# Kernel optimization log

Measured on AMD Instinct MI355X. Metric: run time of the kernel, lower is better.

Reference implementation:

```python
import jax, jax.numpy as jnp
import numpy as np

D_MODEL, NUM_HEADS, ROPE_DIM = 256, 8, 16
B_GRAPHS, N_MAX = 16, 512


def _make_batch():
    # ragged graph sizes between 256 and 512 atoms; contiguous, sorted ids
    sizes = np.array([256 + (i * 256) // 15 for i in range(B_GRAPHS)], dtype=np.int64)
    return np.repeat(np.arange(B_GRAPHS), sizes)  # total N = 6137


def setup_inputs() -> dict:
    key = jax.random.key(0)
    ks = jax.random.split(key, 6)
    batch_np = _make_batch()
    N = int(batch_np.shape[0])
    x = jax.random.normal(ks[0], (N, D_MODEL), jnp.float32)
    pos = jax.random.normal(ks[1], (N, 3), jnp.float32) * 3.0
    W_qkv = jax.random.normal(ks[2], (D_MODEL, 3 * D_MODEL), jnp.float32) / np.sqrt(D_MODEL).astype(np.float32)
    W_out = jax.random.normal(ks[3], (D_MODEL, D_MODEL), jnp.float32) / np.sqrt(D_MODEL).astype(np.float32)
    rope_freqs = jax.random.normal(ks[4], (ROPE_DIM,), jnp.float32) * 0.1
    W_rope = jax.random.normal(ks[5], (ROPE_DIM, NUM_HEADS), jnp.float32) / np.sqrt(ROPE_DIM).astype(np.float32)
    gamma = jnp.ones((D_MODEL,), jnp.float32)
    beta = jnp.zeros((D_MODEL,), jnp.float32)
    return {"x": x, "pos": pos, "batch": jnp.asarray(batch_np, jnp.int32),
            "W_qkv": W_qkv, "W_out": W_out, "rope_freqs": rope_freqs,
            "W_rope": W_rope, "gamma": gamma, "beta": beta,
            "B": B_GRAPHS, "n_max": N_MAX}


def _forward(x, pos, W_qkv, W_out, rope_freqs, W_rope, gamma, beta, batch, B, n_max):
    N, d = x.shape
    H = W_rope.shape[1]
    hd = d // H
    scale = hd ** -0.5
    # pad ragged graphs to [B, n_max] via vectorized scatter (batch is sorted)
    sizes = jax.ops.segment_sum(jnp.ones((N,), jnp.int32), batch, num_segments=B)
    offsets = jnp.concatenate([jnp.zeros((1,), jnp.int32), jnp.cumsum(sizes)[:-1].astype(jnp.int32)])
    pidx = jnp.arange(N, dtype=jnp.int32) - offsets[batch]  # position within graph
    x_pad = jnp.zeros((B, n_max, d), x.dtype).at[batch, pidx].set(x)
    pos_pad = jnp.zeros((B, n_max, 3), pos.dtype).at[batch, pidx].set(pos)
    pad = jnp.ones((B, n_max), bool).at[batch, pidx].set(False)  # True = padding
    # multi-head self-attention on scalar channel
    qkv = x_pad @ W_qkv  # [B, n, 3d]
    q, k, v = jnp.split(qkv, 3, axis=-1)
    heads = lambda t: t.reshape(B, n_max, H, hd).transpose(0, 2, 1, 3)  # [B,H,n,hd]
    q, k, v = heads(q), heads(k), heads(v)
    logits = jnp.einsum('bhid,bhjd->bhij', q, k) * scale
    # Euclidean RoPE distance bias: rope_proj(cos(|omega| * ||r_i - r_j||))
    diff = pos_pad[:, :, None, :] - pos_pad[:, None, :, :]  # [B,n,n,3]
    sq = jnp.sum(diff * diff, axis=-1)
    dist = jnp.where(sq > 0, jnp.sqrt(jnp.where(sq > 0, sq, 1.0)), 0.0)  # safe norm
    fourier = jnp.cos(dist[..., None] * jnp.abs(rope_freqs))  # [B,n,n,r]
    bias = jnp.einsum('bijr,rh->bhij', fourier, W_rope)
    pair_pad = (pad[:, :, None] | pad[:, None, :])[:, None]  # [B,1,n,n]
    bias = jnp.where(pair_pad, 0.0, bias)
    logits = jnp.where(pad[:, None, None, :], -1e9, logits + bias)
    attn = jax.nn.softmax(logits, axis=-1)
    out = jnp.einsum('bhij,bhjd->bhid', attn, v)
    out = out.transpose(0, 2, 1, 3).reshape(B, n_max, d) @ W_out
    out_flat = out[batch, pidx]  # gather back to flat node list
    # residual + LayerNorm (eps = 1e-5)
    y = x + out_flat
    mu = jnp.mean(y, axis=-1, keepdims=True)
    var = jnp.mean((y - mu) ** 2, axis=-1, keepdims=True)
    return gamma * (y - mu) * jax.lax.rsqrt(var + 1e-5) + beta


def reference(x, pos, batch, W_qkv, W_out, rope_freqs, W_rope, gamma, beta, B, n_max):
    return _forward(x, pos, W_qkv, W_out, rope_freqs, W_rope, gamma, beta, batch, B, n_max)
```

## Files before the change

### kernel.cpp

```cpp
#include <hip/hip_runtime.h>
#include <hip/hip_bf16.h>

typedef __hip_bfloat16 bf16;
typedef short bf16x8 __attribute__((ext_vector_type(8)));
typedef float f32x4 __attribute__((ext_vector_type(4)));

#define NGRAPH 16
#define QSCALE 0.17677669529663687f
#define VT_LD 8192

struct __align__(16) bf8x { bf16 v[8]; };

__device__ __forceinline__ float b2f(bf16 v) { return __bfloat162float(v); }

__device__ __forceinline__ bf16x8 ldcvt8(const float* p) {
  float4 u = *(const float4*)p, v = *(const float4*)(p + 4);
  __align__(16) bf16 tmp[8];
  tmp[0] = __float2bfloat16(u.x); tmp[1] = __float2bfloat16(u.y);
  tmp[2] = __float2bfloat16(u.z); tmp[3] = __float2bfloat16(u.w);
  tmp[4] = __float2bfloat16(v.x); tmp[5] = __float2bfloat16(v.y);
  tmp[6] = __float2bfloat16(v.z); tmp[7] = __float2bfloat16(v.w);
  return *(const bf16x8*)tmp;
}

__global__ __launch_bounds__(256) void k_pre(const float* __restrict__ Wqkv,
                                             const float* __restrict__ Wout,
                                             const int* __restrict__ batch,
                                             bf16* __restrict__ Wqkv_t,
                                             bf16* __restrict__ Wout_t,
                                             int* __restrict__ offs, int N) {
  __shared__ float ld[64][65];
  int bid = blockIdx.x, t = threadIdx.x;
  int c = t & 63, r0 = t >> 6;
  if (bid < 48) {
    int k0 = (bid & 3) * 64, n0 = (bid >> 2) * 64;
    #pragma unroll
    for (int r = r0; r < 64; r += 4) ld[r][c] = Wqkv[(size_t)(k0 + r) * 768 + n0 + c];
    __syncthreads();
    #pragma unroll
    for (int r = r0; r < 64; r += 4)
      Wqkv_t[(size_t)(n0 + r) * 256 + k0 + c] = __float2bfloat16(ld[c][r]);
  } else if (bid < 64) {
    int b2 = bid - 48;
    int k0 = (b2 & 3) * 64, n0 = (b2 >> 2) * 64;
    #pragma unroll
    for (int r = r0; r < 64; r += 4) ld[r][c] = Wout[(size_t)(k0 + r) * 256 + n0 + c];
    __syncthreads();
    #pragma unroll
    for (int r = r0; r < 64; r += 4)
      Wout_t[(size_t)(n0 + r) * 256 + k0 + c] = __float2bfloat16(ld[c][r]);
  } else {
    for (int i = t; i < N; i += 256) {
      if (i == 0) { offs[0] = 0; offs[NGRAPH] = N; }
      else if (batch[i] != batch[i - 1]) offs[batch[i]] = i;
    }
  }
}

__global__ __launch_bounds__(256) void k_gemm(const float* __restrict__ x,
                                              const bf16* __restrict__ Wqkv_t,
                                              const int* __restrict__ batch,
                                              const int* __restrict__ offs,
                                              bf16* __restrict__ QKVb,
                                              bf16* __restrict__ VT, int N) {
  __shared__ float tr[64][65];
  __shared__ int rowcol[64];
  int t = threadIdx.x;
  int w = t >> 6, l = t & 63, fr = l & 15, fq = l >> 4;
  int m0 = blockIdx.x * 64, n0 = blockIdx.y * 64;
  if (t < 64) {
    int m = m0 + t; if (m > N - 1) m = N - 1;
    int b = batch[m];
    rowcol[t] = b * 512 + (m - offs[b]);
  }
  int arow = m0 + w * 16 + fr; if (arow > N - 1) arow = N - 1;
  bf16x8 af[8];
  #pragma unroll
  for (int kt = 0; kt < 8; ++kt)
    af[kt] = ldcvt8(x + (size_t)arow * 256 + kt * 32 + fq * 8);
  #pragma unroll
  for (int p = 0; p < 3; ++p) {
    f32x4 acc[4];
    #pragma unroll
    for (int nt = 0; nt < 4; ++nt) {
      acc[nt] = (f32x4){0.f, 0.f, 0.f, 0.f};
      int brow = p * 256 + n0 + nt * 16 + fr;
      #pragma unroll
      for (int kt = 0; kt < 8; ++kt) {
        bf16x8 bf_ = *(const bf16x8*)(Wqkv_t + (size_t)brow * 256 + kt * 32 + fq * 8);
        acc[nt] = __builtin_amdgcn_mfma_f32_16x16x32_bf16(af[kt], bf_, acc[nt], 0, 0, 0);
      }
    }
    float sc = (p == 0) ? QSCALE : 1.f;
    #pragma unroll
    for (int nt = 0; nt < 4; ++nt) {
      int col = p * 256 + n0 + nt * 16 + fr;
      #pragma unroll
      for (int rr = 0; rr < 4; ++rr) {
        int m = m0 + w * 16 + fq * 4 + rr;
        if (m < N) QKVb[(size_t)m * 768 + col] = __float2bfloat16(acc[nt][rr] * sc);
      }
    }
    if (p == 2) {
      #pragma unroll
      for (int nt = 0; nt < 4; ++nt)
        #pragma unroll
        for (int rr = 0; rr < 4; ++rr)
          tr[nt * 16 + fr][w * 16 + fq * 4 + rr] = acc[nt][rr];
      __syncthreads();
      int c = t >> 2, r0 = (t & 3) * 16;
      int dg = n0 + c;
      #pragma unroll
      for (int i = 0; i < 16; ++i) {
        int r = r0 + i;
        VT[(size_t)dg * VT_LD + rowcol[r]] = __float2bfloat16(tr[c][r]);
      }
    }
  }
}

__global__ __launch_bounds__(256) void k_attn(const float* __restrict__ pos,
                                              const float* __restrict__ freqs,
                                              const float* __restrict__ Wrope,
                                              const bf16* __restrict__ QKVb,
                                              const bf16* __restrict__ VT,
                                              const int* __restrict__ offs,
                                              float* __restrict__ Op,
                                              float* __restrict__ lp, int N) {
  __shared__ __align__(16) bf16 Tg[384][8];
  __shared__ __align__(16) bf16 Sbf[2][8][64][8];
  __shared__ __align__(16) bf16 Pt[4][16][40];
  int b = blockIdx.y, jc = blockIdx.z;
  int off = offs[b], n = offs[b + 1] - off;
  int q0 = blockIdx.x * 16;
  if (q0 >= n) return;
  int t = threadIdx.x, w = t >> 6, l = t & 63, fr = l & 15, fq = l >> 4;

  for (int i = t; i < 384; i += 256) {
    float d = i * 0.125f;
    float a[8];
    #pragma unroll
    for (int h = 0; h < 8; ++h) a[h] = 0.f;
    #pragma unroll
    for (int r = 0; r < 16; ++r) {
      float cv = __cosf(d * fabsf(freqs[r]));
      #pragma unroll
      for (int h = 0; h < 8; ++h) a[h] += cv * Wrope[r * 8 + h];
    }
    __align__(16) bf16 row[8];
    #pragma unroll
    for (int h = 0; h < 8; ++h) row[h] = __float2bfloat16(a[h]);
    *(bf16x8*)&Tg[i][0] = *(const bf16x8*)row;
  }

  int h0 = w, h1 = w + 4;
  const bf16* Kb0 = QKVb + (size_t)off * 768 + 256 + h0 * 32 + fq * 8;
  const bf16* Kb1 = QKVb + (size_t)off * 768 + 256 + h1 * 32 + fq * 8;
  const bf16* Vb0 = VT + (size_t)(h0 * 32 + fr) * VT_LD + b * 512 + fq * 8;
  const bf16* Vb1 = VT + (size_t)(h1 * 32 + fr) * VT_LD + b * 512 + fq * 8;
  int qrow = q0 + fr; bool qv = qrow < n;
  size_t qoff = (size_t)(qv ? off + qrow : off) * 768 + fq * 8;
  bf16x8 aq[2];
  aq[0] = *(const bf16x8*)(QKVb + qoff + h0 * 32);
  aq[1] = *(const bf16x8*)(QKVb + qoff + h1 * 32);
  if (!qv) { aq[0] = (bf16x8){0,0,0,0,0,0,0,0}; aq[1] = aq[0]; }

  int bq = t >> 5, bj = t & 31;
  float qpx[2], qpy[2], qpz[2]; bool bqv[2];
  #pragma unroll
  for (int e = 0; e < 2; ++e) {
    int qq = q0 + bq + 8 * e; bqv[e] = qq < n;
    int a = (bqv[e] ? off + qq : off) * 3;
    qpx[e] = pos[a]; qpy[e] = pos[a + 1]; qpz[e] = pos[a + 2];
  }

  f32x4 Oa[2][2];
  Oa[0][0] = (f32x4){0.f,0.f,0.f,0.f}; Oa[0][1] = Oa[0][0];
  Oa[1][0] = Oa[0][0];                 Oa[1][1] = Oa[0][0];
  float lacc[2][4] = {{0.f,0.f,0.f,0.f},{0.f,0.f,0.f,0.f}};
  int jtiles = (n + 31) >> 5;
  int jt0 = (jtiles * jc) >> 1, jt1 = (jtiles * (jc + 1)) >> 1;

  auto produce = [&](int JT, int BUF) {
    int jg = JT * 32 + bj; bool vj = jg < n;
    int a = (vj ? off + jg : off) * 3;
    float jx = pos[a], jy = pos[a + 1], jz = pos[a + 2];
    #pragma unroll
    for (int e = 0; e < 2; ++e) {
      int q = bq + 8 * e;
      int L = (q >> 2) * 16 + (bj & 15);
      int k = (bj >> 4) * 4 + (q & 3);
      if (vj && bqv[e]) {
        float dx = qpx[e] - jx, dy = qpy[e] - jy, dz = qpz[e] - jz;
        float d = sqrtf(dx * dx + dy * dy + dz * dz);
        float fi = d * 8.0f;
        int i = (int)fi; if (i > 382) i = 382;
        float fr2 = fi - (float)i;
        bf8x t0 = *(const bf8x*)&Tg[i][0];
        bf8x t1 = *(const bf8x*)&Tg[i + 1][0];
        #pragma unroll
        for (int h = 0; h < 8; ++h) {
          float u0 = b2f(t0.v[h]);
          float bv = u0 + fr2 * (b2f(t1.v[h]) - u0);
          Sbf[BUF][h][L][k] = __float2bfloat16(bv);
        }
      } else {
        bf16 s = __float2bfloat16(vj ? 0.f : -1e30f);
        #pragma unroll
        for (int h = 0; h < 8; ++h) Sbf[BUF][h][L][k] = s;
      }
    }
  };

  bf16x8 ck[2][2], cv[2][2];
  auto loadt = [&](int JT) {
    int k0 = JT * 32 + fr, k1 = k0 + 16;
    size_t r0 = (size_t)((k0 < n) ? k0 : 0) * 768;
    size_t r1 = (size_t)((k1 < n) ? k1 : 0) * 768;
    ck[0][0] = *(const bf16x8*)(Kb0 + r0); ck[0][1] = *(const bf16x8*)(Kb0 + r1);
    ck[1][0] = *(const bf16x8*)(Kb1 + r0); ck[1][1] = *(const bf16x8*)(Kb1 + r1);
    cv[0][0] = *(const bf16x8*)(Vb0 + JT * 32);
    cv[0][1] = *(const bf16x8*)(Vb0 + (size_t)16 * VT_LD + JT * 32);
    cv[1][0] = *(const bf16x8*)(Vb1 + JT * 32);
    cv[1][1] = *(const bf16x8*)(Vb1 + (size_t)16 * VT_LD + JT * 32);
  };

  __syncthreads();
  produce(jt0, 0);
  __syncthreads();
  for (int jt = jt0; jt < jt1; ++jt) {
    int par = (jt - jt0) & 1;
    loadt(jt);
    if (jt + 1 < jt1) produce(jt + 1, par ^ 1);
    #pragma unroll
    for (int hh = 0; hh < 2; ++hh) {
      int h = w + 4 * hh;
      f32x4 z = {0.f, 0.f, 0.f, 0.f};
      f32x4 S0 = __builtin_amdgcn_mfma_f32_16x16x32_bf16(aq[hh], ck[hh][0], z, 0, 0, 0);
      f32x4 S1 = __builtin_amdgcn_mfma_f32_16x16x32_bf16(aq[hh], ck[hh][1], z, 0, 0, 0);
      bf8x bb = *(const bf8x*)&Sbf[par][h][l][0];
      #pragma unroll
      for (int k = 0; k < 8; ++k) {
        int jti = k >> 2, rr = k & 3;
        float s = (jti ? S1[rr] : S0[rr]) + b2f(bb.v[k]);
        float p = __expf(s);
        lacc[hh][rr] += p;
        Pt[w][fq * 4 + rr][jti * 16 + fr] = __float2bfloat16(p);
      }
      bf16x8 ap = *(const bf16x8*)&Pt[w][fr][fq * 8];
      Oa[hh][0] = __builtin_amdgcn_mfma_f32_16x16x32_bf16(ap, cv[hh][0], Oa[hh][0], 0, 0, 0);
      Oa[hh][1] = __builtin_amdgcn_mfma_f32_16x16x32_bf16(ap, cv[hh][1], Oa[hh][1], 0, 0, 0);
    }
    __syncthreads();
  }
  #pragma unroll
  for (int hh = 0; hh < 2; ++hh)
    #pragma unroll
    for (int rr = 0; rr < 4; ++rr) {
      #pragma unroll
      for (int m2 = 1; m2 <= 8; m2 <<= 1) lacc[hh][rr] += __shfl_xor(lacc[hh][rr], m2);
    }
  float* Opc = Op + (size_t)jc * N * 256;
  float* lpc = lp + (size_t)jc * N * 8;
  #pragma unroll
  for (int hh = 0; hh < 2; ++hh) {
    int h = w + 4 * hh;
    #pragma unroll
    for (int rr = 0; rr < 4; ++rr) {
      int row = q0 + fq * 4 + rr;
      if (row < n) {
        #pragma unroll
        for (int dh = 0; dh < 2; ++dh)
          Opc[(size_t)(off + row) * 256 + h * 32 + dh * 16 + fr] = Oa[hh][dh][rr];
        if (fr == 0) lpc[(size_t)(off + row) * 8 + h] = lacc[hh][rr];
      }
    }
  }
}

__global__ __launch_bounds__(256) void k_out_ln(const float* __restrict__ Op,
                                                const float* __restrict__ lp,
                                                const bf16* __restrict__ Bt,
                                                const float* __restrict__ x,
                                                const float* __restrict__ gamma,
                                                const float* __restrict__ beta,
                                                float* __restrict__ out, int M) {
  __shared__ float ps[4][16], pss[4][16];
  int t = threadIdx.x, w = t >> 6, l = t & 63, fr = l & 15, fq = l >> 4;
  int m0 = blockIdx.x * 16;
  int arow = m0 + fr; if (arow > M - 1) arow = M - 1;
  const float* Op0 = Op;
  const float* Op1 = Op + (size_t)M * 256;
  float linv[8];
  {
    float4 a0 = *(const float4*)(lp + (size_t)arow * 8);
    float4 a1 = *(const float4*)(lp + (size_t)arow * 8 + 4);
    float4 b0 = *(const float4*)(lp + (size_t)(M + arow) * 8);
    float4 b1 = *(const float4*)(lp + (size_t)(M + arow) * 8 + 4);
    linv[0] = 1.f / (a0.x + b0.x); linv[1] = 1.f / (a0.y + b0.y);
    linv[2] = 1.f / (a0.z + b0.z); linv[3] = 1.f / (a0.w + b0.w);
    linv[4] = 1.f / (a1.x + b1.x); linv[5] = 1.f / (a1.y + b1.y);
    linv[6] = 1.f / (a1.z + b1.z); linv[7] = 1.f / (a1.w + b1.w);
  }
  bf16x8 af[8];
  #pragma unroll
  for (int kt = 0; kt < 8; ++kt) {
    size_t o = (size_t)arow * 256 + kt * 32 + fq * 8;
    float4 u0 = *(const float4*)(Op0 + o), v0 = *(const float4*)(Op0 + o + 4);
    float4 u1 = *(const float4*)(Op1 + o), v1 = *(const float4*)(Op1 + o + 4);
    float li = linv[kt];
    __align__(16) bf16 tmp[8];
    tmp[0] = __float2bfloat16((u0.x + u1.x) * li);
    tmp[1] = __float2bfloat16((u0.y + u1.y) * li);
    tmp[2] = __float2bfloat16((u0.z + u1.z) * li);
    tmp[3] = __float2bfloat16((u0.w + u1.w) * li);
    tmp[4] = __float2bfloat16((v0.x + v1.x) * li);
    tmp[5] = __float2bfloat16((v0.y + v1.y) * li);
    tmp[6] = __float2bfloat16((v0.z + v1.z) * li);
    tmp[7] = __float2bfloat16((v0.w + v1.w) * li);
    af[kt] = *(const bf16x8*)tmp;
  }
  f32x4 acc[4];
  #pragma unroll
  for (int nt = 0; nt < 4; ++nt) {
    acc[nt] = (f32x4){0.f, 0.f, 0.f, 0.f};
    int brow = w * 64 + nt * 16 + fr;
    #pragma unroll
    for (int kt = 0; kt < 8; ++kt) {
      bf16x8 bf_ = *(const bf16x8*)(Bt + (size_t)brow * 256 + kt * 32 + fq * 8);
      acc[nt] = __builtin_amdgcn_mfma_f32_16x16x32_bf16(af[kt], bf_, acc[nt], 0, 0, 0);
    }
  }
  float y[4][4];
  #pragma unroll
  for (int rr = 0; rr < 4; ++rr) {
    int row = m0 + fq * 4 + rr;
    int rc = (row < M) ? row : (M - 1);
    float s = 0.f, ss = 0.f;
    #pragma unroll
    for (int nt = 0; nt < 4; ++nt) {
      float v = acc[nt][rr] + x[(size_t)rc * 256 + w * 64 + nt * 16 + fr];
      y[rr][nt] = v; s += v; ss += v * v;
    }
    #pragma unroll
    for (int m2 = 1; m2 <= 8; m2 <<= 1) { s += __shfl_xor(s, m2); ss += __shfl_xor(ss, m2); }
    if (fr == 0) { ps[w][fq * 4 + rr] = s; pss[w][fq * 4 + rr] = ss; }
  }
  __syncthreads();
  #pragma unroll
  for (int rr = 0; rr < 4; ++rr) {
    int row = m0 + fq * 4 + rr;
    int ri = fq * 4 + rr;
    float s = ps[0][ri] + ps[1][ri] + ps[2][ri] + ps[3][ri];
    float ss = pss[0][ri] + pss[1][ri] + pss[2][ri] + pss[3][ri];
    float mean = s * (1.f / 256.f);
    float var = ss * (1.f / 256.f) - mean * mean;
    float rstd = rsqrtf(var + 1e-5f);
    if (row < M) {
      #pragma unroll
      for (int nt = 0; nt < 4; ++nt) {
        int col = w * 64 + nt * 16 + fr;
        out[(size_t)row * 256 + col] = gamma[col] * (y[rr][nt] - mean) * rstd + beta[col];
      }
    }
  }
}

extern "C" void kernel_launch(void* const* d_in, const int* in_sizes, int n_in,
                              void* d_out, int out_size, void* d_ws, size_t ws_size,
                              hipStream_t stream) {
  (void)n_in; (void)out_size; (void)ws_size;
  const float* x     = (const float*)d_in[0];
  const float* pos   = (const float*)d_in[1];
  const int*   batch = (const int*)d_in[2];
  const float* Wqkv  = (const float*)d_in[3];
  const float* Wout  = (const float*)d_in[4];
  const float* freqs = (const float*)d_in[5];
  const float* Wrope = (const float*)d_in[6];
  const float* gamma = (const float*)d_in[7];
  const float* beta  = (const float*)d_in[8];
  float* out = (float*)d_out;

  int N = in_sizes[0] / 256;

  char* base = (char*)d_ws;
  int*   offs   = (int*)base;
  bf16*  QKVb   = (bf16*)(base + 1024);
  bf16*  VT     = (bf16*)(base + 9427456);
  bf16*  Wqkv_t = (bf16*)(base + 13621760);
  bf16*  Wout_t = (bf16*)(base + 14014976);
  float* Op     = (float*)(base + 14146048);
  float* lp     = (float*)(base + 26714624);

  int MBm = (N + 63) / 64;
  k_pre<<<65, 256, 0, stream>>>(Wqkv, Wout, batch, Wqkv_t, Wout_t, offs, N);
  k_gemm<<<dim3(MBm, 4), 256, 0, stream>>>(x, Wqkv_t, batch, offs, QKVb, VT, N);
  k_attn<<<dim3(32, NGRAPH, 2), 256, 0, stream>>>(pos, freqs, Wrope, QKVb, VT, offs, Op, lp, N);
  k_out_ln<<<(N + 15) / 16, 256, 0, stream>>>(Op, lp, Wout_t, x, gamma, beta, out, N);
}
```

Measured before the change: 179.4 us.

## Precompute RoPE bias table once, widen attention key split, shrink GEMM tiles

```diff
diff --git a/kernel.cpp b/kernel.cpp
--- a/kernel.cpp
+++ b/kernel.cpp
@@ -26,8 +26,11 @@
 __global__ __launch_bounds__(256) void k_pre(const float* __restrict__ Wqkv,
                                              const float* __restrict__ Wout,
                                              const int* __restrict__ batch,
+                                             const float* __restrict__ freqs,
+                                             const float* __restrict__ Wrope,
                                              bf16* __restrict__ Wqkv_t,
                                              bf16* __restrict__ Wout_t,
+                                             float* __restrict__ Tblg,
                                              int* __restrict__ offs, int N) {
   __shared__ float ld[64][65];
   int bid = blockIdx.x, t = threadIdx.x;
@@ -49,10 +52,26 @@
     #pragma unroll
     for (int r = r0; r < 64; r += 4)
       Wout_t[(size_t)(n0 + r) * 256 + k0 + c] = __float2bfloat16(ld[c][r]);
-  } else {
+  } else if (bid == 64) {
     for (int i = t; i < N; i += 256) {
       if (i == 0) { offs[0] = 0; offs[NGRAPH] = N; }
       else if (batch[i] != batch[i - 1]) offs[batch[i]] = i;
+    }
+  } else {
+    int i = (bid - 65) * 256 + t;
+    if (i < 384) {
+      float d = i * 0.125f;
+      float a[8];
+      #pragma unroll
+      for (int h = 0; h < 8; ++h) a[h] = 0.f;
+      #pragma unroll
+      for (int r = 0; r < 16; ++r) {
+        float cv = __cosf(d * fabsf(freqs[r]));
+        #pragma unroll
+        for (int h = 0; h < 8; ++h) a[h] += cv * Wrope[r * 8 + h];
+      }
+      #pragma unroll
+      for (int h = 0; h < 8; ++h) Tblg[i * 8 + h] = a[h];
     }
   }
 }
@@ -63,28 +82,29 @@
                                               const int* __restrict__ offs,
                                               bf16* __restrict__ QKVb,
                                               bf16* __restrict__ VT, int N) {
-  __shared__ float tr[64][65];
-  __shared__ int rowcol[64];
+  __shared__ float tr[64][33];
+  __shared__ int rowcol[32];
   int t = threadIdx.x;
   int w = t >> 6, l = t & 63, fr = l & 15, fq = l >> 4;
-  int m0 = blockIdx.x * 64, n0 = blockIdx.y * 64;
-  if (t < 64) {
+  int rh = w & 1, ch = w >> 1;
+  int m0 = blockIdx.x * 32, n0 = blockIdx.y * 64;
+  if (t < 32) {
     int m = m0 + t; if (m > N - 1) m = N - 1;
     int b = batch[m];
     rowcol[t] = b * 512 + (m - offs[b]);
   }
-  int arow = m0 + w * 16 + fr; if (arow > N - 1) arow = N - 1;
+  int arow = m0 + rh * 16 + fr; if (arow > N - 1) arow = N - 1;
   bf16x8 af[8];
   #pragma unroll
   for (int kt = 0; kt < 8; ++kt)
     af[kt] = ldcvt8(x + (size_t)arow * 256 + kt * 32 + fq * 8);
   #pragma unroll
   for (int p = 0; p < 3; ++p) {
-    f32x4 acc[4];
-    #pragma unroll
-    for (int nt = 0; nt < 4; ++nt) {
+    f32x4 acc[2];
+    #pragma unroll
+    for (int nt = 0; nt < 2; ++nt) {
       acc[nt] = (f32x4){0.f, 0.f, 0.f, 0.f};
-      int brow = p * 256 + n0 + nt * 16 + fr;
+      int brow = p * 256 + n0 + ch * 32 + nt * 16 + fr;
       #pragma unroll
       for (int kt = 0; kt < 8; ++kt) {
         bf16x8 bf_ = *(const bf16x8*)(Wqkv_t + (size_t)brow * 256 + kt * 32 + fq * 8);
@@ -93,26 +113,26 @@
     }
     float sc = (p == 0) ? QSCALE : 1.f;
     #pragma unroll
-    for (int nt = 0; nt < 4; ++nt) {
-      int col = p * 256 + n0 + nt * 16 + fr;
+    for (int nt = 0; nt < 2; ++nt) {
+      int col = p * 256 + n0 + ch * 32 + nt * 16 + fr;
       #pragma unroll
       for (int rr = 0; rr < 4; ++rr) {
-        int m = m0 + w * 16 + fq * 4 + rr;
+        int m = m0 + rh * 16 + fq * 4 + rr;
         if (m < N) QKVb[(size_t)m * 768 + col] = __float2bfloat16(acc[nt][rr] * sc);
       }
     }
     if (p == 2) {
       #pragma unroll
-      for (int nt = 0; nt < 4; ++nt)
+      for (int nt = 0; nt < 2; ++nt)
         #pragma unroll
         for (int rr = 0; rr < 4; ++rr)
-          tr[nt * 16 + fr][w * 16 + fq * 4 + rr] = acc[nt][rr];
+          tr[ch * 32 + nt * 16 + fr][rh * 16 + fq * 4 + rr] = acc[nt][rr];
       __syncthreads();
-      int c = t >> 2, r0 = (t & 3) * 16;
+      int c = t >> 2, rr0 = (t & 3) * 8;
       int dg = n0 + c;
       #pragma unroll
-      for (int i = 0; i < 16; ++i) {
-        int r = r0 + i;
+      for (int i = 0; i < 8; ++i) {
+        int r = rr0 + i;
         VT[(size_t)dg * VT_LD + rowcol[r]] = __float2bfloat16(tr[c][r]);
       }
     }
@@ -120,14 +140,13 @@
 }
 
 __global__ __launch_bounds__(256) void k_attn(const float* __restrict__ pos,
-                                              const float* __restrict__ freqs,
-                                              const float* __restrict__ Wrope,
+                                              const float* __restrict__ Tblg,
                                               const bf16* __restrict__ QKVb,
                                               const bf16* __restrict__ VT,
                                               const int* __restrict__ offs,
                                               float* __restrict__ Op,
-                                              float* __restrict__ lp, int N) {
-  __shared__ __align__(16) bf16 Tg[384][8];
+                                              float* __restrict__ lp, int N, int JC) {
+  __shared__ __align__(16) float Tgf[384][8];
   __shared__ __align__(16) bf16 Sbf[2][8][64][8];
   __shared__ __align__(16) bf16 Pt[4][16][40];
   int b = blockIdx.y, jc = blockIdx.z;
@@ -136,21 +155,11 @@
   if (q0 >= n) return;
   int t = threadIdx.x, w = t >> 6, l = t & 63, fr = l & 15, fq = l >> 4;
 
-  for (int i = t; i < 384; i += 256) {
-    float d = i * 0.125f;
-    float a[8];
-    #pragma unroll
-    for (int h = 0; h < 8; ++h) a[h] = 0.f;
-    #pragma unroll
-    for (int r = 0; r < 16; ++r) {
-      float cv = __cosf(d * fabsf(freqs[r]));
-      #pragma unroll
-      for (int h = 0; h < 8; ++h) a[h] += cv * Wrope[r * 8 + h];
-    }
-    __align__(16) bf16 row[8];
-    #pragma unroll
-    for (int h = 0; h < 8; ++h) row[h] = __float2bfloat16(a[h]);
-    *(bf16x8*)&Tg[i][0] = *(const bf16x8*)row;
+  {
+    float4* dst = (float4*)&Tgf[0][0];
+    const float4* src = (const float4*)Tblg;
+    #pragma unroll
+    for (int i = t; i < 768; i += 256) dst[i] = src[i];
   }
 
   int h0 = w, h1 = w + 4;
@@ -179,7 +188,7 @@
   Oa[1][0] = Oa[0][0];                 Oa[1][1] = Oa[0][0];
   float lacc[2][4] = {{0.f,0.f,0.f,0.f},{0.f,0.f,0.f,0.f}};
   int jtiles = (n + 31) >> 5;
-  int jt0 = (jtiles * jc) >> 1, jt1 = (jtiles * (jc + 1)) >> 1;
+  int jt0 = (jtiles * jc) / JC, jt1 = (jtiles * (jc + 1)) / JC;
 
   auto produce = [&](int JT, int BUF) {
     int jg = JT * 32 + bj; bool vj = jg < n;
@@ -196,14 +205,17 @@
         float fi = d * 8.0f;
         int i = (int)fi; if (i > 382) i = 382;
         float fr2 = fi - (float)i;
-        bf8x t0 = *(const bf8x*)&Tg[i][0];
-        bf8x t1 = *(const bf8x*)&Tg[i + 1][0];
-        #pragma unroll
-        for (int h = 0; h < 8; ++h) {
-          float u0 = b2f(t0.v[h]);
-          float bv = u0 + fr2 * (b2f(t1.v[h]) - u0);
-          Sbf[BUF][h][L][k] = __float2bfloat16(bv);
-        }
+        const float* tp = &Tgf[i][0];
+        float4 a0 = *(const float4*)tp,       a1 = *(const float4*)(tp + 4);
+        float4 c0 = *(const float4*)(tp + 8), c1 = *(const float4*)(tp + 12);
+        Sbf[BUF][0][L][k] = __float2bfloat16(a0.x + fr2 * (c0.x - a0.x));
+        Sbf[BUF][1][L][k] = __float2bfloat16(a0.y + fr2 * (c0.y - a0.y));
+        Sbf[BUF][2][L][k] = __float2bfloat16(a0.z + fr2 * (c0.z - a0.z));
+        Sbf[BUF][3][L][k] = __float2bfloat16(a0.w + fr2 * (c0.w - a0.w));
+        Sbf[BUF][4][L][k] = __float2bfloat16(a1.x + fr2 * (c1.x - a1.x));
+        Sbf[BUF][5][L][k] = __float2bfloat16(a1.y + fr2 * (c1.y - a1.y));
+        Sbf[BUF][6][L][k] = __float2bfloat16(a1.z + fr2 * (c1.z - a1.z));
+        Sbf[BUF][7][L][k] = __float2bfloat16(a1.w + fr2 * (c1.w - a1.w));
       } else {
         bf16 s = __float2bfloat16(vj ? 0.f : -1e30f);
         #pragma unroll
@@ -284,40 +296,40 @@
                                                 const float* __restrict__ x,
                                                 const float* __restrict__ gamma,
                                                 const float* __restrict__ beta,
-                                                float* __restrict__ out, int M) {
+                                                float* __restrict__ out, int M, int JC) {
   __shared__ float ps[4][16], pss[4][16];
   int t = threadIdx.x, w = t >> 6, l = t & 63, fr = l & 15, fq = l >> 4;
   int m0 = blockIdx.x * 16;
   int arow = m0 + fr; if (arow > M - 1) arow = M - 1;
-  const float* Op0 = Op;
-  const float* Op1 = Op + (size_t)M * 256;
   float linv[8];
   {
-    float4 a0 = *(const float4*)(lp + (size_t)arow * 8);
-    float4 a1 = *(const float4*)(lp + (size_t)arow * 8 + 4);
-    float4 b0 = *(const float4*)(lp + (size_t)(M + arow) * 8);
-    float4 b1 = *(const float4*)(lp + (size_t)(M + arow) * 8 + 4);
-    linv[0] = 1.f / (a0.x + b0.x); linv[1] = 1.f / (a0.y + b0.y);
-    linv[2] = 1.f / (a0.z + b0.z); linv[3] = 1.f / (a0.w + b0.w);
-    linv[4] = 1.f / (a1.x + b1.x); linv[5] = 1.f / (a1.y + b1.y);
-    linv[6] = 1.f / (a1.z + b1.z); linv[7] = 1.f / (a1.w + b1.w);
+    float ls[8] = {0.f,0.f,0.f,0.f,0.f,0.f,0.f,0.f};
+    for (int c = 0; c < JC; ++c) {
+      const float* p = lp + ((size_t)c * M + arow) * 8;
+      float4 a0 = *(const float4*)p, a1 = *(const float4*)(p + 4);
+      ls[0] += a0.x; ls[1] += a0.y; ls[2] += a0.z; ls[3] += a0.w;
+      ls[4] += a1.x; ls[5] += a1.y; ls[6] += a1.z; ls[7] += a1.w;
+    }
+    #pragma unroll
+    for (int h = 0; h < 8; ++h) linv[h] = 1.f / ls[h];
   }
   bf16x8 af[8];
   #pragma unroll
   for (int kt = 0; kt < 8; ++kt) {
     size_t o = (size_t)arow * 256 + kt * 32 + fq * 8;
-    float4 u0 = *(const float4*)(Op0 + o), v0 = *(const float4*)(Op0 + o + 4);
-    float4 u1 = *(const float4*)(Op1 + o), v1 = *(const float4*)(Op1 + o + 4);
+    float s0 = 0.f, s1 = 0.f, s2 = 0.f, s3 = 0.f, s4 = 0.f, s5 = 0.f, s6 = 0.f, s7 = 0.f;
+    for (int c = 0; c < JC; ++c) {
+      const float* p = Op + (size_t)c * M * 256 + o;
+      float4 u = *(const float4*)p, v = *(const float4*)(p + 4);
+      s0 += u.x; s1 += u.y; s2 += u.z; s3 += u.w;
+      s4 += v.x; s5 += v.y; s6 += v.z; s7 += v.w;
+    }
     float li = linv[kt];
     __align__(16) bf16 tmp[8];
-    tmp[0] = __float2bfloat16((u0.x + u1.x) * li);
-    tmp[1] = __float2bfloat16((u0.y + u1.y) * li);
-    tmp[2] = __float2bfloat16((u0.z + u1.z) * li);
-    tmp[3] = __float2bfloat16((u0.w + u1.w) * li);
-    tmp[4] = __float2bfloat16((v0.x + v1.x) * li);
-    tmp[5] = __float2bfloat16((v0.y + v1.y) * li);
-    tmp[6] = __float2bfloat16((v0.z + v1.z) * li);
-    tmp[7] = __float2bfloat16((v0.w + v1.w) * li);
+    tmp[0] = __float2bfloat16(s0 * li); tmp[1] = __float2bfloat16(s1 * li);
+    tmp[2] = __float2bfloat16(s2 * li); tmp[3] = __float2bfloat16(s3 * li);
+    tmp[4] = __float2bfloat16(s4 * li); tmp[5] = __float2bfloat16(s5 * li);
+    tmp[6] = __float2bfloat16(s6 * li); tmp[7] = __float2bfloat16(s7 * li);
     af[kt] = *(const bf16x8*)tmp;
   }
   f32x4 acc[4];
@@ -369,7 +381,7 @@
 extern "C" void kernel_launch(void* const* d_in, const int* in_sizes, int n_in,
                               void* d_out, int out_size, void* d_ws, size_t ws_size,
                               hipStream_t stream) {
-  (void)n_in; (void)out_size; (void)ws_size;
+  (void)n_in; (void)out_size;
   const float* x     = (const float*)d_in[0];
   const float* pos   = (const float*)d_in[1];
   const int*   batch = (const int*)d_in[2];
@@ -383,18 +395,21 @@
 
   int N = in_sizes[0] / 256;
 
+  int JC = (ws_size >= (size_t)41 * 1024 * 1024) ? 4 : 2;
+
   char* base = (char*)d_ws;
   int*   offs   = (int*)base;
   bf16*  QKVb   = (bf16*)(base + 1024);
   bf16*  VT     = (bf16*)(base + 9427456);
   bf16*  Wqkv_t = (bf16*)(base + 13621760);
   bf16*  Wout_t = (bf16*)(base + 14014976);
-  float* Op     = (float*)(base + 14146048);
-  float* lp     = (float*)(base + 26714624);
-
-  int MBm = (N + 63) / 64;
-  k_pre<<<65, 256, 0, stream>>>(Wqkv, Wout, batch, Wqkv_t, Wout_t, offs, N);
+  float* Tblg   = (float*)(base + 14146048);
+  float* Op     = (float*)(base + 14158336);
+  float* lp     = (float*)(base + 14158336 + (size_t)JC * N * 1024);
+
+  int MBm = (N + 31) / 32;
+  k_pre<<<67, 256, 0, stream>>>(Wqkv, Wout, batch, freqs, Wrope, Wqkv_t, Wout_t, Tblg, offs, N);
   k_gemm<<<dim3(MBm, 4), 256, 0, stream>>>(x, Wqkv_t, batch, offs, QKVb, VT, N);
-  k_attn<<<dim3(32, NGRAPH, 2), 256, 0, stream>>>(pos, freqs, Wrope, QKVb, VT, offs, Op, lp, N);
-  k_out_ln<<<(N + 15) / 16, 256, 0, stream>>>(Op, lp, Wout_t, x, gamma, beta, out, N);
-}
+  k_attn<<<dim3(32, NGRAPH, JC), 256, 0, stream>>>(pos, Tblg, QKVb, VT, offs, Op, lp, N, JC);
+  k_out_ln<<<(N + 15) / 16, 256, 0, stream>>>(Op, lp, Wout_t, x, gamma, beta, out, N, JC);
+}
```

New measurement: 182.8 us. Within noise of the previous version (+1.9%).

## Split attention keys into fixed 128-key chunks and precompute rope-bias table once

Applied to the files above, without the earlier changes.

```diff
diff --git a/kernel.cpp b/kernel.cpp
--- a/kernel.cpp
+++ b/kernel.cpp
@@ -26,8 +26,11 @@
 __global__ __launch_bounds__(256) void k_pre(const float* __restrict__ Wqkv,
                                              const float* __restrict__ Wout,
                                              const int* __restrict__ batch,
+                                             const float* __restrict__ freqs,
+                                             const float* __restrict__ Wrope,
                                              bf16* __restrict__ Wqkv_t,
                                              bf16* __restrict__ Wout_t,
+                                             bf16* __restrict__ Tbg,
                                              int* __restrict__ offs, int N) {
   __shared__ float ld[64][65];
   int bid = blockIdx.x, t = threadIdx.x;
@@ -49,10 +52,28 @@
     #pragma unroll
     for (int r = r0; r < 64; r += 4)
       Wout_t[(size_t)(n0 + r) * 256 + k0 + c] = __float2bfloat16(ld[c][r]);
-  } else {
+  } else if (bid == 64) {
     for (int i = t; i < N; i += 256) {
       if (i == 0) { offs[0] = 0; offs[NGRAPH] = N; }
       else if (batch[i] != batch[i - 1]) offs[batch[i]] = i;
+    }
+  } else {
+    int i = (bid - 65) * 256 + t;
+    if (i < 384) {
+      float d = i * 0.125f;
+      float a[8];
+      #pragma unroll
+      for (int h = 0; h < 8; ++h) a[h] = 0.f;
+      #pragma unroll
+      for (int r = 0; r < 16; ++r) {
+        float cv = __cosf(d * fabsf(freqs[r]));
+        #pragma unroll
+        for (int h = 0; h < 8; ++h) a[h] += cv * Wrope[r * 8 + h];
+      }
+      __align__(16) bf16 row[8];
+      #pragma unroll
+      for (int h = 0; h < 8; ++h) row[h] = __float2bfloat16(a[h]);
+      *(bf16x8*)(Tbg + i * 8) = *(const bf16x8*)row;
     }
   }
 }
@@ -120,8 +141,7 @@
 }
 
 __global__ __launch_bounds__(256) void k_attn(const float* __restrict__ pos,
-                                              const float* __restrict__ freqs,
-                                              const float* __restrict__ Wrope,
+                                              const bf16* __restrict__ Tbg,
                                               const bf16* __restrict__ QKVb,
                                               const bf16* __restrict__ VT,
                                               const int* __restrict__ offs,
@@ -133,25 +153,13 @@
   int b = blockIdx.y, jc = blockIdx.z;
   int off = offs[b], n = offs[b + 1] - off;
   int q0 = blockIdx.x * 16;
-  if (q0 >= n) return;
+  int jtiles = (n + 31) >> 5;
+  int chunks = (jtiles + 3) >> 2;
+  if (q0 >= n || jc >= chunks) return;
   int t = threadIdx.x, w = t >> 6, l = t & 63, fr = l & 15, fq = l >> 4;
 
-  for (int i = t; i < 384; i += 256) {
-    float d = i * 0.125f;
-    float a[8];
-    #pragma unroll
-    for (int h = 0; h < 8; ++h) a[h] = 0.f;
-    #pragma unroll
-    for (int r = 0; r < 16; ++r) {
-      float cv = __cosf(d * fabsf(freqs[r]));
-      #pragma unroll
-      for (int h = 0; h < 8; ++h) a[h] += cv * Wrope[r * 8 + h];
-    }
-    __align__(16) bf16 row[8];
-    #pragma unroll
-    for (int h = 0; h < 8; ++h) row[h] = __float2bfloat16(a[h]);
-    *(bf16x8*)&Tg[i][0] = *(const bf16x8*)row;
-  }
+  for (int i = t; i < 384; i += 256)
+    *(bf16x8*)&Tg[i][0] = *(const bf16x8*)(Tbg + i * 8);
 
   int h0 = w, h1 = w + 4;
   const bf16* Kb0 = QKVb + (size_t)off * 768 + 256 + h0 * 32 + fq * 8;
@@ -178,8 +186,8 @@
   Oa[0][0] = (f32x4){0.f,0.f,0.f,0.f}; Oa[0][1] = Oa[0][0];
   Oa[1][0] = Oa[0][0];                 Oa[1][1] = Oa[0][0];
   float lacc[2][4] = {{0.f,0.f,0.f,0.f},{0.f,0.f,0.f,0.f}};
-  int jtiles = (n + 31) >> 5;
-  int jt0 = (jtiles * jc) >> 1, jt1 = (jtiles * (jc + 1)) >> 1;
+  int jt0 = jc * 4;
+  int jt1 = jt0 + 4; if (jt1 > jtiles) jt1 = jtiles;
 
   auto produce = [&](int JT, int BUF) {
     int jg = JT * 32 + bj; bool vj = jg < n;
@@ -282,6 +290,8 @@
                                                 const float* __restrict__ lp,
                                                 const bf16* __restrict__ Bt,
                                                 const float* __restrict__ x,
+                                                const int* __restrict__ batch,
+                                                const int* __restrict__ offs,
                                                 const float* __restrict__ gamma,
                                                 const float* __restrict__ beta,
                                                 float* __restrict__ out, int M) {
@@ -289,35 +299,38 @@
   int t = threadIdx.x, w = t >> 6, l = t & 63, fr = l & 15, fq = l >> 4;
   int m0 = blockIdx.x * 16;
   int arow = m0 + fr; if (arow > M - 1) arow = M - 1;
-  const float* Op0 = Op;
-  const float* Op1 = Op + (size_t)M * 256;
+  int bg = batch[arow];
+  int ng = offs[bg + 1] - offs[bg];
+  int chunksL = (((ng + 31) >> 5) + 3) >> 2;
   float linv[8];
   {
-    float4 a0 = *(const float4*)(lp + (size_t)arow * 8);
-    float4 a1 = *(const float4*)(lp + (size_t)arow * 8 + 4);
-    float4 b0 = *(const float4*)(lp + (size_t)(M + arow) * 8);
-    float4 b1 = *(const float4*)(lp + (size_t)(M + arow) * 8 + 4);
-    linv[0] = 1.f / (a0.x + b0.x); linv[1] = 1.f / (a0.y + b0.y);
-    linv[2] = 1.f / (a0.z + b0.z); linv[3] = 1.f / (a0.w + b0.w);
-    linv[4] = 1.f / (a1.x + b1.x); linv[5] = 1.f / (a1.y + b1.y);
-    linv[6] = 1.f / (a1.z + b1.z); linv[7] = 1.f / (a1.w + b1.w);
+    float ls[8] = {0.f,0.f,0.f,0.f,0.f,0.f,0.f,0.f};
+    for (int c = 0; c < chunksL; ++c) {
+      const float* p = lp + ((size_t)c * M + arow) * 8;
+      float4 a0 = *(const float4*)p, a1 = *(const float4*)(p + 4);
+      ls[0] += a0.x; ls[1] += a0.y; ls[2] += a0.z; ls[3] += a0.w;
+      ls[4] += a1.x; ls[5] += a1.y; ls[6] += a1.z; ls[7] += a1.w;
+    }
+    #pragma unroll
+    for (int h = 0; h < 8; ++h) linv[h] = 1.f / ls[h];
   }
   bf16x8 af[8];
   #pragma unroll
   for (int kt = 0; kt < 8; ++kt) {
     size_t o = (size_t)arow * 256 + kt * 32 + fq * 8;
-    float4 u0 = *(const float4*)(Op0 + o), v0 = *(const float4*)(Op0 + o + 4);
-    float4 u1 = *(const float4*)(Op1 + o), v1 = *(const float4*)(Op1 + o + 4);
+    float s0 = 0.f, s1 = 0.f, s2 = 0.f, s3 = 0.f, s4 = 0.f, s5 = 0.f, s6 = 0.f, s7 = 0.f;
+    for (int c = 0; c < chunksL; ++c) {
+      const float* p = Op + (size_t)c * M * 256 + o;
+      float4 u = *(const float4*)p, v = *(const float4*)(p + 4);
+      s0 += u.x; s1 += u.y; s2 += u.z; s3 += u.w;
+      s4 += v.x; s5 += v.y; s6 += v.z; s7 += v.w;
+    }
     float li = linv[kt];
     __align__(16) bf16 tmp[8];
-    tmp[0] = __float2bfloat16((u0.x + u1.x) * li);
-    tmp[1] = __float2bfloat16((u0.y + u1.y) * li);
-    tmp[2] = __float2bfloat16((u0.z + u1.z) * li);
-    tmp[3] = __float2bfloat16((u0.w + u1.w) * li);
-    tmp[4] = __float2bfloat16((v0.x + v1.x) * li);
-    tmp[5] = __float2bfloat16((v0.y + v1.y) * li);
-    tmp[6] = __float2bfloat16((v0.z + v1.z) * li);
-    tmp[7] = __float2bfloat16((v0.w + v1.w) * li);
+    tmp[0] = __float2bfloat16(s0 * li); tmp[1] = __float2bfloat16(s1 * li);
+    tmp[2] = __float2bfloat16(s2 * li); tmp[3] = __float2bfloat16(s3 * li);
+    tmp[4] = __float2bfloat16(s4 * li); tmp[5] = __float2bfloat16(s5 * li);
+    tmp[6] = __float2bfloat16(s6 * li); tmp[7] = __float2bfloat16(s7 * li);
     af[kt] = *(const bf16x8*)tmp;
   }
   f32x4 acc[4];
@@ -389,12 +402,13 @@
   bf16*  VT     = (bf16*)(base + 9427456);
   bf16*  Wqkv_t = (bf16*)(base + 13621760);
   bf16*  Wout_t = (bf16*)(base + 14014976);
-  float* Op     = (float*)(base + 14146048);
-  float* lp     = (float*)(base + 26714624);
+  bf16*  Tbg    = (bf16*)(base + 14146048);
+  float* Op     = (float*)(base + 14152448);
+  float* lp     = (float*)(base + 39289600);
 
   int MBm = (N + 63) / 64;
-  k_pre<<<65, 256, 0, stream>>>(Wqkv, Wout, batch, Wqkv_t, Wout_t, offs, N);
+  k_pre<<<67, 256, 0, stream>>>(Wqkv, Wout, batch, freqs, Wrope, Wqkv_t, Wout_t, Tbg, offs, N);
   k_gemm<<<dim3(MBm, 4), 256, 0, stream>>>(x, Wqkv_t, batch, offs, QKVb, VT, N);
-  k_attn<<<dim3(32, NGRAPH, 2), 256, 0, stream>>>(pos, freqs, Wrope, QKVb, VT, offs, Op, lp, N);
-  k_out_ln<<<(N + 15) / 16, 256, 0, stream>>>(Op, lp, Wout_t, x, gamma, beta, out, N);
-}
+  k_attn<<<dim3(32, NGRAPH, 4), 256, 0, stream>>>(pos, Tbg, QKVb, VT, offs, Op, lp, N);
+  k_out_ln<<<(N + 15) / 16, 256, 0, stream>>>(Op, lp, Wout_t, x, batch, offs, gamma, beta, out, N);
+}
```

Measured after the change: 183.0 us. About the same (+2.0%).
